# Performance work log

Hardware: AMD Instinct MI355X
Metric: run time of the kernel (lower is better)

Reference implementation:

```python
import jax, jax.numpy as jnp
import numpy as np
import math

NUM_HEADS = 16
TOPK = 64
EMBED = 1024

def setup_inputs() -> dict:
    key = jax.random.key(0)
    ks = jax.random.split(key, 11)
    b, s, e = 2, 2048, EMBED
    scale = 1.0 / math.sqrt(e)
    inp = {
        'q': jax.random.normal(ks[0], (b, s, e), dtype=jnp.float32),
        'k': jax.random.normal(ks[1], (b, s, e), dtype=jnp.float32),
        'v': jax.random.normal(ks[2], (b, s, e), dtype=jnp.float32),
        'Wq': jax.random.normal(ks[3], (e, e), dtype=jnp.float32) * scale,
        'bq': jnp.zeros((e,), dtype=jnp.float32),
        'Wk': jax.random.normal(ks[4], (e, e), dtype=jnp.float32) * scale,
        'bk': jnp.zeros((e,), dtype=jnp.float32),
        'Wv': jax.random.normal(ks[5], (e, e), dtype=jnp.float32) * scale,
        'bv': jnp.zeros((e,), dtype=jnp.float32),
        'Wo': jax.random.normal(ks[6], (e, e), dtype=jnp.float32) * scale,
        'bo': jnp.zeros((e,), dtype=jnp.float32),
    }
    return inp

def _topk_attention(Q, K, V, topk):
    # Q,K,V: (b, h, s, d)
    d = Q.shape[-1]
    scores = jnp.einsum('bhqd,bhkd->bhqk', Q, K) / jnp.sqrt(jnp.asarray(d, Q.dtype))
    topk_scores, topk_idx = jax.lax.top_k(scores, topk)  # (b,h,s,topk)
    probs = jax.nn.softmax(topk_scores, axis=-1)
    # gather V rows per (b,h): V_bh[idx] -> (s, topk, d); avoids (b,h,s,s,d) expand
    gather = jax.vmap(jax.vmap(lambda Vbh, idx: Vbh[idx]))
    sel = gather(V, topk_idx)  # (b,h,s,topk,d)
    return jnp.einsum('bhqk,bhqkd->bhqd', probs, sel)

def reference(q, k, v, Wq, bq, Wk, bk, Wv, bv, Wo, bo):
    b, s, e = q.shape
    h = NUM_HEADS
    d = e // h
    # NOTE: original torch code reshapes (b, s, e) -> (b, h, s, d) directly (no transpose)
    Q = (q @ Wq.T + bq).reshape(b, h, s, d)
    K = (k @ Wk.T + bk).reshape(b, h, s, d)
    V = (v @ Wv.T + bv).reshape(b, h, s, d)
    attn = _topk_attention(Q, K, V, TOPK)  # (b,h,s,d)
    out = attn.reshape(b, s, e)
    return out @ Wo.T + bo
```

## Files before the change

kernel.cpp:

```cpp
#include <hip/hip_runtime.h>
#include <stdint.h>

using u8  = unsigned char;
using s8  = signed char;
using u16 = unsigned short;
using u32 = unsigned int;
using u64 = unsigned long long;

typedef int   v4i __attribute__((ext_vector_type(4)));
typedef float v4f __attribute__((ext_vector_type(4)));
typedef short v8s __attribute__((ext_vector_type(8)));

__device__ __forceinline__ u16 f2bf(float f){
  u32 u = __builtin_bit_cast(u32, f);
  u32 r = (u + 0x7FFFu + ((u >> 16) & 1u)) >> 16;
  return (u16)r;
}
__device__ __forceinline__ float bf2f(u16 b){
  u32 u = ((u32)b) << 16;
  return __builtin_bit_cast(float, u);
}

__global__ __launch_bounds__(256) void quant_digits(
    const float* __restrict__ in, s8* __restrict__ dig, int n, float scale, float clampv)
{
  int t = blockIdx.x * 256 + threadIdx.x;
  int n8 = n >> 3;
  if (t >= n8) return;
  const float4* inv = (const float4*)in;
  float4 a = inv[2*t], b = inv[2*t+1];
  float xs[8] = {a.x,a.y,a.z,a.w,b.x,b.y,b.z,b.w};
  u64 p0=0,p1=0,p2=0,p3=0;
#pragma unroll
  for (int j=0;j<8;j++){
    float xv = fminf(fmaxf(xs[j], -clampv), clampv);
    int X = (int)rintf(xv * scale);
    int d0 = (int)(s8)(X & 255); X = (X - d0) >> 8;
    int d1 = (int)(s8)(X & 255); X = (X - d1) >> 8;
    int d2 = (int)(s8)(X & 255); X = (X - d2) >> 8;
    int d3 = X;
    p0 |= ((u64)(u8)(s8)d0) << (8*j);
    p1 |= ((u64)(u8)(s8)d1) << (8*j);
    p2 |= ((u64)(u8)(s8)d2) << (8*j);
    p3 |= ((u64)(u8)(s8)d3) << (8*j);
  }
  u64* o = (u64*)dig;
  size_t np8 = (size_t)n8;
  o[t] = p0; o[np8 + t] = p1; o[2*np8 + t] = p2; o[3*np8 + t] = p3;
}

#define MFMA_I8(c, a, b) asm volatile("v_mfma_i32_16x16x64_i8 %0, %1, %2, %0" : "+v"(c) : "v"(a), "v"(b))

__global__ __launch_bounds__(256) void gemm_i8(
    const s8* __restrict__ Ad, const s8* __restrict__ Wd, const float* __restrict__ bias,
    double* __restrict__ Cd, u16* __restrict__ Cb)
{
  __shared__ alignas(16) s8 As[4][32][80];
  __shared__ alignas(16) s8 Bs[4][32][80];
  const int i0 = blockIdx.x * 32, o0 = blockIdx.y * 32;
  const int t = threadIdx.x, w = t >> 6, lane = t & 63;
  const int wr = w >> 1, wc = w & 1, l15 = lane & 15, lg = lane >> 4;
  const size_t APL = 4194304, WPL = 1048576;

  v4i c1={0,0,0,0}, c2={0,0,0,0}, c3={0,0,0,0}, c4={0,0,0,0};

  for (int kt = 0; kt < 16; ++kt){
#pragma unroll
    for (int j = 0; j < 2; ++j){
      int cid = t*2 + j;
      int p = cid >> 7, rem = cid & 127;
      int row = rem >> 2, c16 = (rem & 3) << 4;
      int4 av = *(const int4*)(Ad + (size_t)p*APL + (size_t)(i0+row)*1024 + kt*64 + c16);
      *(int4*)&As[p][row][c16] = av;
      int4 bv = *(const int4*)(Wd + (size_t)p*WPL + (size_t)(o0+row)*1024 + kt*64 + c16);
      *(int4*)&Bs[p][row][c16] = bv;
    }
    __syncthreads();
    v4i a0 = *(const v4i*)&As[0][wr*16+l15][lg*16];
    v4i a1 = *(const v4i*)&As[1][wr*16+l15][lg*16];
    v4i a2 = *(const v4i*)&As[2][wr*16+l15][lg*16];
    v4i a3 = *(const v4i*)&As[3][wr*16+l15][lg*16];
    v4i b0 = *(const v4i*)&Bs[0][wc*16+l15][lg*16];
    v4i b1 = *(const v4i*)&Bs[1][wc*16+l15][lg*16];
    v4i b2 = *(const v4i*)&Bs[2][wc*16+l15][lg*16];
    v4i b3 = *(const v4i*)&Bs[3][wc*16+l15][lg*16];
    MFMA_I8(c1, a0, b3); MFMA_I8(c1, a1, b2); MFMA_I8(c1, a2, b1); MFMA_I8(c1, a3, b0);
    MFMA_I8(c2, a1, b3); MFMA_I8(c2, a2, b2); MFMA_I8(c2, a3, b1);
    MFMA_I8(c3, a2, b3); MFMA_I8(c3, a3, b2);
    MFMA_I8(c4, a3, b3);
    __syncthreads();
  }
  const int oc = o0 + wc*16 + l15;
  const double bv = (double)bias[oc];
#pragma unroll
  for (int e = 0; e < 4; ++e){
    double val = (double)c1[e]*0x1p-35 + (double)c2[e]*0x1p-27
               + (double)c3[e]*0x1p-19 + (double)c4[e]*0x1p-11 + bv;
    int orow = i0 + wr*16 + lg*4 + e;
    size_t idx = (size_t)orow*1024 + oc;
    Cd[idx] = val;
    Cb[idx] = f2bf((float)val);
  }
}

template<int ABF16, int OUTBF>
__global__ __launch_bounds__(256) void gemm_bf16k(
    const void* __restrict__ Ap, const float* __restrict__ W, const float* __restrict__ bias,
    void* __restrict__ C)
{
  __shared__ alignas(16) u16 As[32][72];
  __shared__ alignas(16) u16 Bs[32][72];
  const int i0 = blockIdx.x * 32, o0 = blockIdx.y * 32;
  const int t = threadIdx.x, w = t >> 6, lane = t & 63;
  const int wr = w >> 1, wc = w & 1, l15 = lane & 15, lg = lane >> 4;
  const int row = t >> 3, c8 = (t & 7) * 8;
  v4f acc = {0.f,0.f,0.f,0.f};
  for (int kt = 0; kt < 16; ++kt){
    if (ABF16){
      v8s x = *(const v8s*)((const u16*)Ap + (size_t)(i0+row)*1024 + kt*64 + c8);
      *(v8s*)&As[row][c8] = x;
    } else {
      const float* A = (const float*)Ap;
      const float4 x0 = *(const float4*)(A + (size_t)(i0+row)*1024 + kt*64 + c8);
      const float4 x1 = *(const float4*)(A + (size_t)(i0+row)*1024 + kt*64 + c8 + 4);
      v8s pk;
      pk[0]=(short)f2bf(x0.x); pk[1]=(short)f2bf(x0.y); pk[2]=(short)f2bf(x0.z); pk[3]=(short)f2bf(x0.w);
      pk[4]=(short)f2bf(x1.x); pk[5]=(short)f2bf(x1.y); pk[6]=(short)f2bf(x1.z); pk[7]=(short)f2bf(x1.w);
      *(v8s*)&As[row][c8] = pk;
    }
    {
      const float4 y0 = *(const float4*)(W + (size_t)(o0+row)*1024 + kt*64 + c8);
      const float4 y1 = *(const float4*)(W + (size_t)(o0+row)*1024 + kt*64 + c8 + 4);
      v8s pk;
      pk[0]=(short)f2bf(y0.x); pk[1]=(short)f2bf(y0.y); pk[2]=(short)f2bf(y0.z); pk[3]=(short)f2bf(y0.w);
      pk[4]=(short)f2bf(y1.x); pk[5]=(short)f2bf(y1.y); pk[6]=(short)f2bf(y1.z); pk[7]=(short)f2bf(y1.w);
      *(v8s*)&Bs[row][c8] = pk;
    }
    __syncthreads();
    v8s a0 = *(const v8s*)&As[wr*16+l15][lg*8];
    v8s a1 = *(const v8s*)&As[wr*16+l15][lg*8+32];
    v8s b0 = *(const v8s*)&Bs[wc*16+l15][lg*8];
    v8s b1 = *(const v8s*)&Bs[wc*16+l15][lg*8+32];
    acc = __builtin_amdgcn_mfma_f32_16x16x32_bf16(a0, b0, acc, 0, 0, 0);
    acc = __builtin_amdgcn_mfma_f32_16x16x32_bf16(a1, b1, acc, 0, 0, 0);
    __syncthreads();
  }
  const int oc = o0 + wc*16 + l15;
  const float bvv = bias[oc];
#pragma unroll
  for (int e=0;e<4;e++){
    int orow = i0 + wr*16 + lg*4 + e;
    size_t idx = (size_t)orow*1024 + oc;
    if (OUTBF) ((u16*)C)[idx] = f2bf(acc[e] + bvv);
    else       ((float*)C)[idx] = acc[e] + bvv;
  }
}

#define CCAP 192
__global__ __launch_bounds__(512, 4) void attn_topk(
    const u16* __restrict__ Qb, const u16* __restrict__ Kb,
    const double* __restrict__ Qd, const double* __restrict__ Kd,
    const u16* __restrict__ Vb, u16* __restrict__ Ab, u32* __restrict__ flags)
{
  __shared__ u32 candL[32*CCAP];
  __shared__ u32 selpL[16*64];
  __shared__ int cntA[32];

  const int lid = blockIdx.y * 64 + blockIdx.x;
  const int bh  = (lid & 7) * 4 + (lid >> 9);
  const int qb  = (lid >> 3) & 63;
  const size_t base = (size_t)(bh >> 4) * 2097152 + (size_t)(bh & 15) * 131072;
  const int q0 = qb * 32;
  const int tid = threadIdx.x, w = tid >> 6, lane = tid & 63;
  const int l15 = lane & 15, lg = lane >> 4;
  const u64 ltmask = (1ull << lane) - 1ull;

  if (tid < 32) cntA[tid] = 0;
  __syncthreads();

  const v4f vzero = {0.f,0.f,0.f,0.f};
  float nrmA, nrmB;
  {
    const size_t qoffA = base + (size_t)(q0 + l15)*64 + lg*8;
    v8s aA0 = *(const v8s*)(Qb + qoffA);
    v8s aA1 = *(const v8s*)(Qb + qoffA + 32);
    v8s aB0 = *(const v8s*)(Qb + qoffA + 1024);
    v8s aB1 = *(const v8s*)(Qb + qoffA + 1024 + 32);

    nrmA = 0.f; nrmB = 0.f;
#pragma unroll
    for (int m = 0; m < 8; ++m){
      float xA0 = bf2f((u16)aA0[m]), xA1 = bf2f((u16)aA1[m]);
      float xB0 = bf2f((u16)aB0[m]), xB1 = bf2f((u16)aB1[m]);
      nrmA = fmaf(xA0,xA0,nrmA); nrmA = fmaf(xA1,xA1,nrmA);
      nrmB = fmaf(xB0,xB0,nrmB); nrmB = fmaf(xB1,xB1,nrmB);
    }
    nrmA += __shfl_xor(nrmA,16); nrmA += __shfl_xor(nrmA,32);
    nrmB += __shfl_xor(nrmB,16); nrmB += __shfl_xor(nrmB,32);
    float T0A[4], T0B[4];
#pragma unroll
    for (int e = 0; e < 4; ++e){
      T0A[e] = 0.2f * sqrtf(__shfl(nrmA, lg*4 + e));
      T0B[e] = 0.2f * sqrtf(__shfl(nrmB, lg*4 + e));
    }

    const u16* Kw = Kb + base + (size_t)(w*256 + l15)*64 + lg*8;
    v8s b0 = *(const v8s*)(Kw);
    v8s b1 = *(const v8s*)(Kw + 32);

    auto step = [&](int kt, v8s b0c, v8s b1c){
      v4f sA = __builtin_amdgcn_mfma_f32_16x16x32_bf16(aA0, b0c, vzero, 0,0,0);
      sA = __builtin_amdgcn_mfma_f32_16x16x32_bf16(aA1, b1c, sA, 0,0,0);
      v4f sB = __builtin_amdgcn_mfma_f32_16x16x32_bf16(aB0, b0c, vzero, 0,0,0);
      sB = __builtin_amdgcn_mfma_f32_16x16x32_bf16(aB1, b1c, sB, 0,0,0);
      const u32 col = (u32)(w*256 + kt*16 + l15);
#pragma unroll
      for (int e = 0; e < 4; ++e){
        float sc = sA[e]*0.125f;
        if (sc >= T0A[e]){
          int row = lg*4 + e;
          int pos = atomicAdd(&cntA[row], 1);
          if (pos < CCAP) candL[row*CCAP + pos] = ((u32)f2bf(sc)<<16) | col;
        }
        float sc2 = sB[e]*0.125f;
        if (sc2 >= T0B[e]){
          int row = 16 + lg*4 + e;
          int pos = atomicAdd(&cntA[row], 1);
          if (pos < CCAP) candL[row*CCAP + pos] = ((u32)f2bf(sc2)<<16) | col;
        }
      }
    };

    for (int kt = 0; kt < 15; ++kt){
      v8s n0 = *(const v8s*)(Kw + (size_t)(kt+1)*1024);
      v8s n1 = *(const v8s*)(Kw + (size_t)(kt+1)*1024 + 32);
      step(kt, b0, b1);
      b0 = n0; b1 = n1;
    }
    step(15, b0, b1);
  }
  __syncthreads();

  for (int pass = 0; pass < 2; ++pass){
    const int R0 = pass*16 + w*2;
    const float nrmP0 = (pass == 0) ? nrmA : nrmB;
    u32 pk0[2], pk1[2], pk2[2], cstore[2], tv[2];
    bool fail[2];

#pragma unroll
    for (int rr = 0; rr < 2; ++rr){
      const int R = R0 + rr;
      int craw = cntA[R];
      fail[rr] = (craw > CCAP);
      cstore[rr] = (u32)(craw > CCAP ? CCAP : craw);
#pragma unroll
      for (int s = 0; s < 3; ++s){
        u32 idx = (u32)(64*s + lane);
        u32 val = (idx < cstore[rr]) ? candL[R*CCAP + idx] : 0u;
        if (s == 0) pk0[rr] = val; else if (s == 1) pk1[rr] = val; else pk2[rr] = val;
      }
      tv[rr] = 0u;
    }

    for (int bit = 14; bit >= 0; --bit){
#pragma unroll
      for (int rr = 0; rr < 2; ++rr){
        u32 tt = tv[rr] | (1u << bit);
        int c = (int)__popcll(__ballot((pk0[rr] >> 16) >= tt))
              + (int)__popcll(__ballot((pk1[rr] >> 16) >= tt))
              + (int)__popcll(__ballot((pk2[rr] >> 16) >= tt));
        if (c >= 64) tv[rr] = tt;
      }
    }

    int na[2], nb[2];
#pragma unroll
    for (int rr = 0; rr < 2; ++rr){
      const int R = R0 + rr;
      const int Rl = R & 15;
      float t64f = bf2f((u16)tv[rr]);
      float T0R = 0.2f * sqrtf(__shfl(nrmP0, R & 15));
      float thi = t64f + 0.052f, tlo = t64f - 0.052f;
      int a_ = 0, b_ = 0;
#pragma unroll
      for (int s = 0; s < 3; ++s){
        u32 pkv = (s == 0) ? pk0[rr] : ((s == 1) ? pk1[rr] : pk2[rr]);
        bool act = (u32)(64*s + lane) < cstore[rr];
        float v = bf2f((u16)(pkv >> 16));
        bool aut = act && (v > thi);
        bool ban = act && !aut && (v >= tlo);
        u64 ma = __ballot(aut);
        if (aut){
          int pos = a_ + (int)__popcll(ma & ltmask);
          if (pos < 64) selpL[Rl*64 + pos] = pkv;
        }
        a_ += (int)__popcll(ma);
        u64 mb = __ballot(ban);
        if (ban){
          int pos = b_ + (int)__popcll(mb & ltmask);
          if (pos < 64) candL[R*CCAP + pos] = pkv;
        }
        b_ += (int)__popcll(mb);
      }
      bool fl = fail[rr] || (t64f < T0R + 0.055f) || (t64f >= 3.98f) || (b_ > 64);
      fail[rr] = fl;
      if (lane == 0) flags[bh*2048 + q0 + R] = fl ? 1u : 0u;
      na[rr] = fl ? 64 : (a_ > 64 ? 64 : a_);
      nb[rr] = fl ? 0  : b_;
    }
    asm volatile("s_waitcnt lgkmcnt(0)" ::: "memory");
    __builtin_amdgcn_sched_barrier(0);

    const double* Kdh = Kd + base;
    const double* Qdh = Qd + base + (size_t)q0*64;
    u32 bpk[2];
#pragma unroll
    for (int rr = 0; rr < 2; ++rr)
      bpk[rr] = (lane < nb[rr]) ? candL[(R0+rr)*CCAP + lane] : 0u;
    double ac0[2] = {0,0}, ac1[2] = {0,0};
#pragma unroll 4
    for (int j = 0; j < 32; ++j){
#pragma unroll
      for (int rr = 0; rr < 2; ++rr){
        double2 kv = ((const double2*)(Kdh + (size_t)(bpk[rr] & 0x7FFu)*64))[j];
        double2 qv = ((const double2*)(Qdh + (size_t)(R0+rr)*64))[j];
        ac0[rr] = fma(qv.x, kv.x, ac0[rr]);
        ac1[rr] = fma(qv.y, kv.y, ac1[rr]);
      }
    }
    double mv[2]; int mi[2];
#pragma unroll
    for (int rr = 0; rr < 2; ++rr){
      mv[rr] = (lane < nb[rr]) ? (ac0[rr] + ac1[rr]) : -1.0e300;
      mi[rr] = (lane < nb[rr]) ? (int)(bpk[rr] & 0x7FFu) : 0x7FFFFFFF;
    }
    int maxnb = nb[0] > nb[1] ? nb[0] : nb[1];
    int rank[2] = {0,0};
    for (int j = 0; j < maxnb; ++j){
#pragma unroll
      for (int rr = 0; rr < 2; ++rr){
        double ov = __shfl(mv[rr], j); int oi = __shfl(mi[rr], j);
        rank[rr] += (ov > mv[rr] || (ov == mv[rr] && oi < mi[rr])) ? 1 : 0;
      }
    }
#pragma unroll
    for (int rr = 0; rr < 2; ++rr){
      int need = 64 - na[rr]; if (need > nb[rr]) need = nb[rr];
      if (lane < nb[rr] && rank[rr] < need)
        selpL[((R0+rr) & 15)*64 + na[rr] + rank[rr]] = bpk[rr];
    }
    asm volatile("s_waitcnt lgkmcnt(0)" ::: "memory");
    __builtin_amdgcn_sched_barrier(0);

    u32 sidx[2]; float scv[2], pp[2];
#pragma unroll
    for (int rr = 0; rr < 2; ++rr){
      u32 pr = selpL[((R0+rr) & 15)*64 + lane];
      sidx[rr] = pr & 0x7FFu;
      scv[rr] = __builtin_bit_cast(float, pr & 0xFFFF0000u);
    }
#pragma unroll
    for (int rr = 0; rr < 2; ++rr){
      float mx = scv[rr];
#pragma unroll
      for (int off = 32; off; off >>= 1) mx = fmaxf(mx, __shfl_xor(mx, off));
      float p = expf(scv[rr] - mx);
      float Z = p;
#pragma unroll
      for (int off = 32; off; off >>= 1) Z += __shfl_xor(Z, off);
      pp[rr] = p / Z;
    }
    u64 myp0 = ((u64)__builtin_bit_cast(u32, pp[0]) << 32) | (u64)sidx[0];
    u64 myp1 = ((u64)__builtin_bit_cast(u32, pp[1]) << 32) | (u64)sidx[1];

    const int h = lane >> 5, dl = lane & 31;
    float u0[2] = {0,0}, u1[2] = {0,0};
#pragma unroll 4
    for (int j = 0; j < 64; j += 2){
      u64 pr0 = __shfl(myp0, j + h);
      u64 pr1 = __shfl(myp1, j + h);
#pragma unroll
      for (int rr = 0; rr < 2; ++rr){
        u64 pr = (rr == 0) ? pr0 : pr1;
        float pv = __builtin_bit_cast(float, (u32)(pr >> 32));
        u32 vv = *(const u32*)(Vb + base + (size_t)((u32)pr & 0x7FFu)*64 + 2*dl);
        u0[rr] = fmaf(pv, bf2f((u16)(vv & 0xFFFFu)), u0[rr]);
        u1[rr] = fmaf(pv, bf2f((u16)(vv >> 16)),     u1[rr]);
      }
    }
#pragma unroll
    for (int rr = 0; rr < 2; ++rr){
      u0[rr] += __shfl_xor(u0[rr], 32);
      u1[rr] += __shfl_xor(u1[rr], 32);
    }
    if (lane < 32){
#pragma unroll
      for (int rr = 0; rr < 2; ++rr){
        u32 o = (u32)f2bf(u0[rr]) | ((u32)f2bf(u1[rr]) << 16);
        *(u32*)(Ab + base + (size_t)(q0 + R0 + rr)*64 + 2*dl) = o;
      }
    }
  }
}

__global__ __launch_bounds__(256) void attn_fallback(
    const u32* __restrict__ flags, const double* __restrict__ Qd,
    const double* __restrict__ Kd, const u16* __restrict__ Vb,
    u16* __restrict__ Ab)
{
  __shared__ double ktileL[4][16*64];
  __shared__ double valsL[2048];
  __shared__ double qlds[64];
  __shared__ double selvL[64];
  __shared__ int    seliL[64];
  __shared__ float  ppL[64];
  __shared__ float  ovL[4][64];
  __shared__ double redv[4];
  __shared__ int    redi[4];
  __shared__ double bcv;
  __shared__ int    bci;
  __shared__ u32    mskL;

  const int blk = blockIdx.x;
  const int tid = threadIdx.x, w = tid >> 6, lane = tid & 63;

  if (tid == 0){
    u32 m = 0;
    for (int i = 0; i < 16; ++i) m |= (flags[blk*16 + i] ? 1u : 0u) << i;
    mskL = m;
  }
  __syncthreads();
  const u32 msk = mskL;
  if (msk == 0u) return;

  for (int i = 0; i < 16; ++i){
    if (!((msk >> i) & 1u)) continue;
    const int g = blk*16 + i;
    const int bh = g >> 11, qrow = g & 2047;
    const size_t base = (size_t)(bh >> 4)*2097152 + (size_t)(bh & 15)*131072;
    if (tid < 64) qlds[tid] = Qd[base + (size_t)qrow*64 + tid];
    __syncthreads();

    double* ktw = ktileL[w];
    const int gg = lane >> 4, r = lane & 15;
    for (int t = 0; t < 32; ++t){
      const int k0 = w*512 + t*16;
#pragma unroll
      for (int r2 = 0; r2 < 16; ++r2)
        ktw[r2*64 + ((lane + r2) & 63)] = Kd[base + (size_t)(k0 + r2)*64 + lane];
      double p = 0.0;
#pragma unroll
      for (int dd = 0; dd < 16; ++dd){
        int d = gg*16 + dd;
        p = fma(qlds[d], ktw[r*64 + ((d + r) & 63)], p);
      }
      p += __shfl_xor(p, 16);
      p += __shfl_xor(p, 32);
      if (lane < 16) valsL[k0 + lane] = p * 0.125;
    }
    __syncthreads();

    double myv[8];
#pragma unroll
    for (int m2 = 0; m2 < 8; ++m2) myv[m2] = valsL[tid*8 + m2];

    double pvv = 1.0e300; int pii = -1;
    for (int step = 0; step < 64; ++step){
      double bv = -1.0e300; int bi = 0x7FFFFFFF;
#pragma unroll
      for (int m2 = 0; m2 < 8; ++m2){
        double vv = myv[m2]; int col = tid*8 + m2;
        bool after = (vv < pvv) || (vv == pvv && col > pii);
        bool bet = after && (vv > bv || (vv == bv && col < bi));
        bv = bet ? vv : bv; bi = bet ? col : bi;
      }
#pragma unroll
      for (int off = 32; off; off >>= 1){
        double ov = __shfl_xor(bv, off); int oi = __shfl_xor(bi, off);
        bool tk = (ov > bv) || (ov == bv && oi < bi);
        bv = tk ? ov : bv; bi = tk ? oi : bi;
      }
      if (lane == 0){ redv[w] = bv; redi[w] = bi; }
      __syncthreads();
      if (tid == 0){
        double fv = redv[0]; int fi = redi[0];
#pragma unroll
        for (int x = 1; x < 4; ++x){
          bool tk = (redv[x] > fv) || (redv[x] == fv && redi[x] < fi);
          fv = tk ? redv[x] : fv; fi = tk ? redi[x] : fi;
        }
        bcv = fv; bci = fi; selvL[step] = fv; seliL[step] = fi;
      }
      __syncthreads();
      pvv = bcv; pii = bci;
    }

    if (w == 0){
      float sc = (float)selvL[lane];
      float mx = sc;
#pragma unroll
      for (int off = 32; off; off >>= 1) mx = fmaxf(mx, __shfl_xor(mx, off));
      float p = expf(sc - mx);
      float Z = p;
#pragma unroll
      for (int off = 32; off; off >>= 1) Z += __shfl_xor(Z, off);
      ppL[lane] = p / Z;
    }
    __syncthreads();

    float o = 0.f;
#pragma unroll
    for (int j = 0; j < 16; ++j){
      int jj = w*16 + j;
      o = fmaf(ppL[jj], bf2f(Vb[base + (size_t)seliL[jj]*64 + lane]), o);
    }
    ovL[w][lane] = o;
    __syncthreads();
    if (w == 0){
      float oo = (ovL[0][lane] + ovL[1][lane]) + (ovL[2][lane] + ovL[3][lane]);
      Ab[base + (size_t)qrow*64 + lane] = f2bf(oo);
    }
    __syncthreads();
  }
}

extern "C" void kernel_launch(void* const* d_in, const int* in_sizes, int n_in,
                              void* d_out, int out_size, void* d_ws, size_t ws_size,
                              hipStream_t stream)
{
  (void)in_sizes; (void)n_in; (void)out_size; (void)ws_size;
  const float* q  = (const float*)d_in[0];
  const float* k  = (const float*)d_in[1];
  const float* v  = (const float*)d_in[2];
  const float* Wq = (const float*)d_in[3];
  const float* bq = (const float*)d_in[4];
  const float* Wk = (const float*)d_in[5];
  const float* bk = (const float*)d_in[6];
  const float* Wv = (const float*)d_in[7];
  const float* bv = (const float*)d_in[8];
  const float* Wo = (const float*)d_in[9];
  const float* bo = (const float*)d_in[10];

  char* ws = (char*)d_ws;
  const size_t MB = 1048576;
  double* Qd  = (double*)(ws);
  double* Kd  = (double*)(ws + 32*MB);
  u16*    Qb  = (u16*)  (ws + 64*MB);
  u16*    Kb  = (u16*)  (ws + 72*MB);
  u16*    Abf = (u16*)  (ws + 80*MB);
  s8*     dact= (s8*)   (ws + 88*MB);
  u16*    Vbf = (u16*)  (ws + 88*MB);
  s8*     dw  = (s8*)   (ws + 104*MB);
  u32*    flg = (u32*)  (ws + 104*MB);

  quant_digits<<<2048, 256, 0, stream>>>(q,  dact, 4194304, 134217728.0f, 7.75f);
  quant_digits<<<512,  256, 0, stream>>>(Wq, dw,   1048576, 4294967296.0f, 0.2495f);
  gemm_i8<<<dim3(128, 32), 256, 0, stream>>>(dact, dw, bq, Qd, Qb);
  quant_digits<<<2048, 256, 0, stream>>>(k,  dact, 4194304, 134217728.0f, 7.75f);
  quant_digits<<<512,  256, 0, stream>>>(Wk, dw,   1048576, 4294967296.0f, 0.2495f);
  gemm_i8<<<dim3(128, 32), 256, 0, stream>>>(dact, dw, bk, Kd, Kb);
  gemm_bf16k<0,1><<<dim3(128, 32), 256, 0, stream>>>(v, Wv, bv, Vbf);
  attn_topk<<<dim3(64, 32), 512, 0, stream>>>(Qb, Kb, Qd, Kd, Vbf, Abf, flg);
  attn_fallback<<<4096, 256, 0, stream>>>(flg, Qd, Kd, Vbf, Abf);
  gemm_bf16k<1,0><<<dim3(128, 32), 256, 0, stream>>>(Abf, Wo, bo, d_out);
}
```

Before: 660.4 us.

## Enlarge GEMM block tiles to 64x64 with 2x2 MFMA subtiles per wave

```diff
diff --git a/kernel.cpp b/kernel.cpp
--- a/kernel.cpp
+++ b/kernel.cpp
@@ -55,52 +55,72 @@
     const s8* __restrict__ Ad, const s8* __restrict__ Wd, const float* __restrict__ bias,
     double* __restrict__ Cd, u16* __restrict__ Cb)
 {
-  __shared__ alignas(16) s8 As[4][32][80];
-  __shared__ alignas(16) s8 Bs[4][32][80];
-  const int i0 = blockIdx.x * 32, o0 = blockIdx.y * 32;
+  __shared__ alignas(16) s8 As[4][64][80];
+  __shared__ alignas(16) s8 Bs[4][64][80];
+  const int i0 = blockIdx.x * 64, o0 = blockIdx.y * 64;
   const int t = threadIdx.x, w = t >> 6, lane = t & 63;
   const int wr = w >> 1, wc = w & 1, l15 = lane & 15, lg = lane >> 4;
+  const int sr = (t >> 2) & 63, sc = (t & 3) << 4;
   const size_t APL = 4194304, WPL = 1048576;
 
-  v4i c1={0,0,0,0}, c2={0,0,0,0}, c3={0,0,0,0}, c4={0,0,0,0};
+  v4i acc[2][2][4];
+#pragma unroll
+  for (int tr = 0; tr < 2; ++tr)
+#pragma unroll
+    for (int tc = 0; tc < 2; ++tc)
+#pragma unroll
+      for (int c = 0; c < 4; ++c) acc[tr][tc][c] = (v4i){0,0,0,0};
 
   for (int kt = 0; kt < 16; ++kt){
 #pragma unroll
-    for (int j = 0; j < 2; ++j){
-      int cid = t*2 + j;
-      int p = cid >> 7, rem = cid & 127;
-      int row = rem >> 2, c16 = (rem & 3) << 4;
-      int4 av = *(const int4*)(Ad + (size_t)p*APL + (size_t)(i0+row)*1024 + kt*64 + c16);
-      *(int4*)&As[p][row][c16] = av;
-      int4 bv = *(const int4*)(Wd + (size_t)p*WPL + (size_t)(o0+row)*1024 + kt*64 + c16);
-      *(int4*)&Bs[p][row][c16] = bv;
-    }
-    __syncthreads();
-    v4i a0 = *(const v4i*)&As[0][wr*16+l15][lg*16];
-    v4i a1 = *(const v4i*)&As[1][wr*16+l15][lg*16];
-    v4i a2 = *(const v4i*)&As[2][wr*16+l15][lg*16];
-    v4i a3 = *(const v4i*)&As[3][wr*16+l15][lg*16];
-    v4i b0 = *(const v4i*)&Bs[0][wc*16+l15][lg*16];
-    v4i b1 = *(const v4i*)&Bs[1][wc*16+l15][lg*16];
-    v4i b2 = *(const v4i*)&Bs[2][wc*16+l15][lg*16];
-    v4i b3 = *(const v4i*)&Bs[3][wc*16+l15][lg*16];
-    MFMA_I8(c1, a0, b3); MFMA_I8(c1, a1, b2); MFMA_I8(c1, a2, b1); MFMA_I8(c1, a3, b0);
-    MFMA_I8(c2, a1, b3); MFMA_I8(c2, a2, b2); MFMA_I8(c2, a3, b1);
-    MFMA_I8(c3, a2, b3); MFMA_I8(c3, a3, b2);
-    MFMA_I8(c4, a3, b3);
+    for (int p = 0; p < 4; ++p){
+      int4 av = *(const int4*)(Ad + (size_t)p*APL + (size_t)(i0+sr)*1024 + kt*64 + sc);
+      *(int4*)&As[p][sr][sc] = av;
+      int4 bv = *(const int4*)(Wd + (size_t)p*WPL + (size_t)(o0+sr)*1024 + kt*64 + sc);
+      *(int4*)&Bs[p][sr][sc] = bv;
+    }
+    __syncthreads();
+    v4i af[2][4], bf[2][4];
+#pragma unroll
+    for (int tr = 0; tr < 2; ++tr)
+#pragma unroll
+      for (int p = 0; p < 4; ++p){
+        af[tr][p] = *(const v4i*)&As[p][wr*32 + tr*16 + l15][lg*16];
+        bf[tr][p] = *(const v4i*)&Bs[p][wc*32 + tr*16 + l15][lg*16];
+      }
+#pragma unroll
+    for (int tr = 0; tr < 2; ++tr)
+#pragma unroll
+      for (int tc = 0; tc < 2; ++tc){
+        MFMA_I8(acc[tr][tc][0], af[tr][0], bf[tc][3]);
+        MFMA_I8(acc[tr][tc][0], af[tr][1], bf[tc][2]);
+        MFMA_I8(acc[tr][tc][0], af[tr][2], bf[tc][1]);
+        MFMA_I8(acc[tr][tc][0], af[tr][3], bf[tc][0]);
+        MFMA_I8(acc[tr][tc][1], af[tr][1], bf[tc][3]);
+        MFMA_I8(acc[tr][tc][1], af[tr][2], bf[tc][2]);
+        MFMA_I8(acc[tr][tc][1], af[tr][3], bf[tc][1]);
+        MFMA_I8(acc[tr][tc][2], af[tr][2], bf[tc][3]);
+        MFMA_I8(acc[tr][tc][2], af[tr][3], bf[tc][2]);
+        MFMA_I8(acc[tr][tc][3], af[tr][3], bf[tc][3]);
+      }
     __syncthreads();
   }
-  const int oc = o0 + wc*16 + l15;
-  const double bv = (double)bias[oc];
-#pragma unroll
-  for (int e = 0; e < 4; ++e){
-    double val = (double)c1[e]*0x1p-35 + (double)c2[e]*0x1p-27
-               + (double)c3[e]*0x1p-19 + (double)c4[e]*0x1p-11 + bv;
-    int orow = i0 + wr*16 + lg*4 + e;
-    size_t idx = (size_t)orow*1024 + oc;
-    Cd[idx] = val;
-    Cb[idx] = f2bf((float)val);
-  }
+#pragma unroll
+  for (int tr = 0; tr < 2; ++tr)
+#pragma unroll
+    for (int tc = 0; tc < 2; ++tc){
+      const int oc = o0 + wc*32 + tc*16 + l15;
+      const double bv = (double)bias[oc];
+#pragma unroll
+      for (int e = 0; e < 4; ++e){
+        double val = (double)acc[tr][tc][0][e]*0x1p-35 + (double)acc[tr][tc][1][e]*0x1p-27
+                   + (double)acc[tr][tc][2][e]*0x1p-19 + (double)acc[tr][tc][3][e]*0x1p-11 + bv;
+        int orow = i0 + wr*32 + tr*16 + lg*4 + e;
+        size_t idx = (size_t)orow*1024 + oc;
+        Cd[idx] = val;
+        Cb[idx] = f2bf((float)val);
+      }
+    }
 }
 
 template<int ABF16, int OUTBF>
@@ -108,52 +128,85 @@
     const void* __restrict__ Ap, const float* __restrict__ W, const float* __restrict__ bias,
     void* __restrict__ C)
 {
-  __shared__ alignas(16) u16 As[32][72];
-  __shared__ alignas(16) u16 Bs[32][72];
-  const int i0 = blockIdx.x * 32, o0 = blockIdx.y * 32;
+  __shared__ alignas(16) u16 As[64][72];
+  __shared__ alignas(16) u16 Bs[64][72];
+  const int i0 = blockIdx.x * 64, o0 = blockIdx.y * 64;
   const int t = threadIdx.x, w = t >> 6, lane = t & 63;
   const int wr = w >> 1, wc = w & 1, l15 = lane & 15, lg = lane >> 4;
-  const int row = t >> 3, c8 = (t & 7) * 8;
-  v4f acc = {0.f,0.f,0.f,0.f};
+  const int sr = t >> 2, sc = (t & 3) << 4;
+
+  v4f acc[2][2];
+#pragma unroll
+  for (int tr = 0; tr < 2; ++tr)
+#pragma unroll
+    for (int tc = 0; tc < 2; ++tc) acc[tr][tc] = (v4f){0.f,0.f,0.f,0.f};
+
   for (int kt = 0; kt < 16; ++kt){
     if (ABF16){
-      v8s x = *(const v8s*)((const u16*)Ap + (size_t)(i0+row)*1024 + kt*64 + c8);
-      *(v8s*)&As[row][c8] = x;
+      const u16* A = (const u16*)Ap;
+      v8s x0 = *(const v8s*)(A + (size_t)(i0+sr)*1024 + kt*64 + sc);
+      v8s x1 = *(const v8s*)(A + (size_t)(i0+sr)*1024 + kt*64 + sc + 8);
+      *(v8s*)&As[sr][sc] = x0;
+      *(v8s*)&As[sr][sc+8] = x1;
     } else {
       const float* A = (const float*)Ap;
-      const float4 x0 = *(const float4*)(A + (size_t)(i0+row)*1024 + kt*64 + c8);
-      const float4 x1 = *(const float4*)(A + (size_t)(i0+row)*1024 + kt*64 + c8 + 4);
-      v8s pk;
-      pk[0]=(short)f2bf(x0.x); pk[1]=(short)f2bf(x0.y); pk[2]=(short)f2bf(x0.z); pk[3]=(short)f2bf(x0.w);
-      pk[4]=(short)f2bf(x1.x); pk[5]=(short)f2bf(x1.y); pk[6]=(short)f2bf(x1.z); pk[7]=(short)f2bf(x1.w);
-      *(v8s*)&As[row][c8] = pk;
+      v8s pk0, pk1;
+#pragma unroll
+      for (int h = 0; h < 2; ++h){
+        const float4 y0 = *(const float4*)(A + (size_t)(i0+sr)*1024 + kt*64 + sc + h*8);
+        const float4 y1 = *(const float4*)(A + (size_t)(i0+sr)*1024 + kt*64 + sc + h*8 + 4);
+        v8s& pk = h ? pk1 : pk0;
+        pk[0]=(short)f2bf(y0.x); pk[1]=(short)f2bf(y0.y); pk[2]=(short)f2bf(y0.z); pk[3]=(short)f2bf(y0.w);
+        pk[4]=(short)f2bf(y1.x); pk[5]=(short)f2bf(y1.y); pk[6]=(short)f2bf(y1.z); pk[7]=(short)f2bf(y1.w);
+      }
+      *(v8s*)&As[sr][sc] = pk0;
+      *(v8s*)&As[sr][sc+8] = pk1;
     }
     {
-      const float4 y0 = *(const float4*)(W + (size_t)(o0+row)*1024 + kt*64 + c8);
-      const float4 y1 = *(const float4*)(W + (size_t)(o0+row)*1024 + kt*64 + c8 + 4);
-      v8s pk;
-      pk[0]=(short)f2bf(y0.x); pk[1]=(short)f2bf(y0.y); pk[2]=(short)f2bf(y0.z); pk[3]=(short)f2bf(y0.w);
-      pk[4]=(short)f2bf(y1.x); pk[5]=(short)f2bf(y1.y); pk[6]=(short)f2bf(y1.z); pk[7]=(short)f2bf(y1.w);
-      *(v8s*)&Bs[row][c8] = pk;
-    }
-    __syncthreads();
-    v8s a0 = *(const v8s*)&As[wr*16+l15][lg*8];
-    v8s a1 = *(const v8s*)&As[wr*16+l15][lg*8+32];
-    v8s b0 = *(const v8s*)&Bs[wc*16+l15][lg*8];
-    v8s b1 = *(const v8s*)&Bs[wc*16+l15][lg*8+32];
-    acc = __builtin_amdgcn_mfma_f32_16x16x32_bf16(a0, b0, acc, 0, 0, 0);
-    acc = __builtin_amdgcn_mfma_f32_16x16x32_bf16(a1, b1, acc, 0, 0, 0);
+      v8s pk0, pk1;
+#pragma unroll
+      for (int h = 0; h < 2; ++h){
+        const float4 y0 = *(const float4*)(W + (size_t)(o0+sr)*1024 + kt*64 + sc + h*8);
+        const float4 y1 = *(const float4*)(W + (size_t)(o0+sr)*1024 + kt*64 + sc + h*8 + 4);
+        v8s& pk = h ? pk1 : pk0;
+        pk[0]=(short)f2bf(y0.x); pk[1]=(short)f2bf(y0.y); pk[2]=(short)f2bf(y0.z); pk[3]=(short)f2bf(y0.w);
+        pk[4]=(short)f2bf(y1.x); pk[5]=(short)f2bf(y1.y); pk[6]=(short)f2bf(y1.z); pk[7]=(short)f2bf(y1.w);
+      }
+      *(v8s*)&Bs[sr][sc] = pk0;
+      *(v8s*)&Bs[sr][sc+8] = pk1;
+    }
+    __syncthreads();
+    v8s a[2][2], b[2][2];
+#pragma unroll
+    for (int tr = 0; tr < 2; ++tr)
+#pragma unroll
+      for (int ks = 0; ks < 2; ++ks){
+        a[tr][ks] = *(const v8s*)&As[wr*32 + tr*16 + l15][ks*32 + lg*8];
+        b[tr][ks] = *(const v8s*)&Bs[wc*32 + tr*16 + l15][ks*32 + lg*8];
+      }
+#pragma unroll
+    for (int tr = 0; tr < 2; ++tr)
+#pragma unroll
+      for (int tc = 0; tc < 2; ++tc){
+        acc[tr][tc] = __builtin_amdgcn_mfma_f32_16x16x32_bf16(a[tr][0], b[tc][0], acc[tr][tc], 0, 0, 0);
+        acc[tr][tc] = __builtin_amdgcn_mfma_f32_16x16x32_bf16(a[tr][1], b[tc][1], acc[tr][tc], 0, 0, 0);
+      }
     __syncthreads();
   }
-  const int oc = o0 + wc*16 + l15;
-  const float bvv = bias[oc];
-#pragma unroll
-  for (int e=0;e<4;e++){
-    int orow = i0 + wr*16 + lg*4 + e;
-    size_t idx = (size_t)orow*1024 + oc;
-    if (OUTBF) ((u16*)C)[idx] = f2bf(acc[e] + bvv);
-    else       ((float*)C)[idx] = acc[e] + bvv;
-  }
+#pragma unroll
+  for (int tr = 0; tr < 2; ++tr)
+#pragma unroll
+    for (int tc = 0; tc < 2; ++tc){
+      const int oc = o0 + wc*32 + tc*16 + l15;
+      const float bvv = bias[oc];
+#pragma unroll
+      for (int e = 0; e < 4; ++e){
+        int orow = i0 + wr*32 + tr*16 + lg*4 + e;
+        size_t idx = (size_t)orow*1024 + oc;
+        if (OUTBF) ((u16*)C)[idx] = f2bf(acc[tr][tc][e] + bvv);
+        else       ((float*)C)[idx] = acc[tr][tc][e] + bvv;
+      }
+    }
 }
 
 #define CCAP 192
@@ -555,12 +608,12 @@
 
   quant_digits<<<2048, 256, 0, stream>>>(q,  dact, 4194304, 134217728.0f, 7.75f);
   quant_digits<<<512,  256, 0, stream>>>(Wq, dw,   1048576, 4294967296.0f, 0.2495f);
-  gemm_i8<<<dim3(128, 32), 256, 0, stream>>>(dact, dw, bq, Qd, Qb);
+  gemm_i8<<<dim3(64, 16), 256, 0, stream>>>(dact, dw, bq, Qd, Qb);
   quant_digits<<<2048, 256, 0, stream>>>(k,  dact, 4194304, 134217728.0f, 7.75f);
   quant_digits<<<512,  256, 0, stream>>>(Wk, dw,   1048576, 4294967296.0f, 0.2495f);
-  gemm_i8<<<dim3(128, 32), 256, 0, stream>>>(dact, dw, bk, Kd, Kb);
-  gemm_bf16k<0,1><<<dim3(128, 32), 256, 0, stream>>>(v, Wv, bv, Vbf);
+  gemm_i8<<<dim3(64, 16), 256, 0, stream>>>(dact, dw, bk, Kd, Kb);
+  gemm_bf16k<0,1><<<dim3(64, 16), 256, 0, stream>>>(v, Wv, bv, Vbf);
   attn_topk<<<dim3(64, 32), 512, 0, stream>>>(Qb, Kb, Qd, Kd, Vbf, Abf, flg);
   attn_fallback<<<4096, 256, 0, stream>>>(flg, Qd, Kd, Vbf, Abf);
-  gemm_bf16k<1,0><<<dim3(128, 32), 256, 0, stream>>>(Abf, Wo, bo, d_out);
-}
+  gemm_bf16k<1,0><<<dim3(64, 16), 256, 0, stream>>>(Abf, Wo, bo, d_out);
+}
```

New measurement: 588.4 us. 1.12x faster.
